# Kernel tuning notes

Measured on AMD Instinct MI355X. Metric: run time of the kernel, lower is better.

Reference implementation:

```python
import jax, jax.numpy as jnp
import numpy as np

B, T, J = 8, 1024, 25
D_MODEL, D_STATE, D_CONV, EXPAND = 256, 16, 4, 2
D_INNER = EXPAND * D_MODEL            # 512
DT_RANK = (D_MODEL + 15) // 16        # 16
N_CLASSES = 60


def layernorm(x, g, b, eps=1e-5):
    mu = x.mean(-1, keepdims=True)
    var = ((x - mu) ** 2).mean(-1, keepdims=True)
    return (x - mu) * jax.lax.rsqrt(var + eps) * g + b


def selective_scan(u, delta, A, Bm, Cm, D):
    # u, delta: [b,l,d]; A: [d,n]; Bm, Cm: [b,l,n]; D: [d]
    dA = jnp.exp(delta[..., None] * A)                              # [b,l,d,n]
    dBu = delta[..., None] * Bm[:, :, None, :] * u[..., None]        # [b,l,d,n]

    def step(h, inp):
        dA_t, dBu_t, C_t = inp
        h = dA_t * h + dBu_t                                         # [b,d,n]
        y = jnp.einsum('bdn,bn->bd', h, C_t)
        return h, y

    h0 = jnp.zeros((u.shape[0], u.shape[2], A.shape[1]), u.dtype)
    _, ys = jax.lax.scan(step, h0, (jnp.moveaxis(dA, 1, 0),
                                    jnp.moveaxis(dBu, 1, 0),
                                    jnp.moveaxis(Cm, 1, 0)))
    return jnp.moveaxis(ys, 0, 1) + u * D                            # [b,l,d]


def setup_inputs() -> dict:
    key = jax.random.key(0)
    ks = jax.random.split(key, 12)
    rn = lambda k, s, sc=0.02: jax.random.normal(k, s, jnp.float32) * sc
    A_log = jnp.log(jnp.tile(jnp.arange(1, D_STATE + 1, dtype=jnp.float32), (D_INNER, 1)))
    return {
        'x': jax.random.normal(ks[0], (B, T, J, 3), jnp.float32),
        'embed_w': rn(ks[1], (D_MODEL, J * 9)), 'embed_b': jnp.zeros((D_MODEL,), jnp.float32),
        'pre_g': jnp.ones((D_MODEL,), jnp.float32), 'pre_b': jnp.zeros((D_MODEL,), jnp.float32),
        'in_proj_w': rn(ks[2], (2 * D_INNER, D_MODEL)),
        'conv_w': rn(ks[3], (D_INNER, 1, D_CONV)), 'conv_b': jnp.zeros((D_INNER,), jnp.float32),
        'x_proj_w': rn(ks[4], (DT_RANK + 2 * D_STATE, D_INNER)),
        'dt_proj_w': rn(ks[5], (D_INNER, DT_RANK)), 'dt_proj_b': rn(ks[6], (D_INNER,), 0.1),
        'A_log': A_log, 'D': jnp.ones((D_INNER,), jnp.float32),
        'out_proj_w': rn(ks[7], (D_MODEL, D_INNER)),
        'post_g': jnp.ones((D_MODEL,), jnp.float32), 'post_b': jnp.zeros((D_MODEL,), jnp.float32),
        'fine_w': rn(ks[8], (N_CLASSES, D_MODEL)), 'fine_b': jnp.zeros((N_CLASSES,), jnp.float32),
    }


def reference(x, embed_w, embed_b, pre_g, pre_b, in_proj_w, conv_w, conv_b,
              x_proj_w, dt_proj_w, dt_proj_b, A_log, D, out_proj_w,
              post_g, post_b, fine_w, fine_b):
    b, t = x.shape[0], x.shape[1]
    # --- SkeletonNormalizer: root-center (scale_joints=None) ---
    pos = x[..., :3] - x[:, :, 0:1, :3]                              # [B,T,J,3]
    # --- MotionFeatureBuilder: pos / vel / acc ---
    vel = jnp.concatenate([jnp.zeros_like(pos[:, :1]), pos[:, 1:] - pos[:, :-1]], axis=1)
    acc = jnp.concatenate([jnp.zeros_like(vel[:, :1]), vel[:, 1:] - vel[:, :-1]], axis=1)
    feat = jnp.concatenate([pos, vel, acc], axis=-1).reshape(b, t, -1)  # [B,T,J*9]
    # --- embed ---
    feat = feat @ embed_w.T + embed_b                                # [B,T,D_MODEL]
    # --- Mamba block on pre-norm, residual add ---
    hn = layernorm(feat, pre_g, pre_b)
    xz = hn @ in_proj_w.T                                            # [B,T,2*D_INNER]
    xm, res = jnp.split(xz, 2, axis=-1)
    # depthwise causal conv1d over time
    xm = jax.lax.conv_general_dilated(
        jnp.swapaxes(xm, 1, 2), conv_w, (1,), [(D_CONV - 1, 0)],
        dimension_numbers=('NCH', 'OIH', 'NCH'), feature_group_count=D_INNER)
    xm = jnp.swapaxes(xm + conv_b[None, :, None], 1, 2)              # [B,T,D_INNER]
    xm = jax.nn.silu(xm)
    dbl = xm @ x_proj_w.T                                            # [B,T,DT_RANK+2*D_STATE]
    dt = dbl[..., :DT_RANK]
    Bm = dbl[..., DT_RANK:DT_RANK + D_STATE]
    Cm = dbl[..., DT_RANK + D_STATE:]
    delta = jax.nn.softplus(dt @ dt_proj_w.T + dt_proj_b)            # [B,T,D_INNER]
    A = -jnp.exp(A_log)                                              # [D_INNER,D_STATE]
    y = selective_scan(xm, delta, A, Bm, Cm, D)
    y = y * jax.nn.silu(res)
    y = y @ out_proj_w.T                                             # [B,T,D_MODEL]
    feat = feat + y
    # --- post norm, mean pool, classify ---
    feat = layernorm(feat, post_g, post_b)
    pooled = feat.mean(axis=1)                                       # [B,D_MODEL]
    return pooled @ fine_w.T + fine_b                                # [B,N_CLASSES]
```

## Files before the change

### kernel.cpp

```cpp
#include <hip/hip_runtime.h>
#include <hip/hip_bf16.h>
#include <math.h>

#define Bb 8
#define Tt 1024
#define Jj 25
#define D_MODEL 256
#define D_STATE 16
#define D_CONV 4
#define D_INNER 512
#define DT_RANK 16
#define N_CLASSES 60
#define Mrows (Bb*Tt)
#define NC 64
#define CL 16

typedef unsigned short u16;
using bf16x8 = __attribute__((ext_vector_type(8))) __bf16;
using f32x4  = __attribute__((ext_vector_type(4))) float;

__device__ inline u16 f2bf(float x) {
    unsigned u = __float_as_uint(x);
    unsigned r = (u + 0x7fffu + ((u >> 16) & 1u)) >> 16;
    return (u16)r;
}
__device__ inline float bf2f(u16 h) { return __uint_as_float((unsigned)h << 16); }
__device__ inline void split2(float x, u16& h, u16& l) {
    h = f2bf(x);
    l = f2bf(x - bf2f(h));
}
__device__ inline float softplus_fast(float s) {
    return fmaxf(s, 0.f) + __logf(1.f + __expf(-fabsf(s)));
}
__device__ inline f32x4 mfma3(bf16x8 ah, bf16x8 al, bf16x8 bh, bf16x8 bl, f32x4 c) {
    c = __builtin_amdgcn_mfma_f32_16x16x32_bf16(al, bh, c, 0, 0, 0);
    c = __builtin_amdgcn_mfma_f32_16x16x32_bf16(ah, bl, c, 0, 0, 0);
    c = __builtin_amdgcn_mfma_f32_16x16x32_bf16(ah, bh, c, 0, 0, 0);
    return c;
}

__global__ __launch_bounds__(256) void prep_kernel(
    const float* __restrict__ ew, const float* __restrict__ iw,
    const float* __restrict__ xw, const float* __restrict__ ow,
    u16* __restrict__ ebh, u16* __restrict__ ebl,
    u16* __restrict__ iph, u16* __restrict__ ipl,
    u16* __restrict__ xph, u16* __restrict__ xpl,
    u16* __restrict__ oph, u16* __restrict__ opl,
    float* __restrict__ blockpart) {
    int blk = blockIdx.x;
    if (blk < 1888) {
        int i = blk * 256 + threadIdx.x;
        const float* src; u16 *dh, *dl; int K, kshift, idx;
        if (i < 65536)       { src = ew; dh = ebh; dl = ebl; K = 225; kshift = 8; idx = i; }
        else if (i < 327680) { src = iw; dh = iph; dl = ipl; K = 256; kshift = 8; idx = i - 65536; }
        else if (i < 352256) { src = xw; dh = xph; dl = xpl; K = 512; kshift = 9; idx = i - 327680; }
        else                 { src = ow; dh = oph; dl = opl; K = 512; kshift = 9; idx = i - 352256; }
        int n = idx >> kshift;
        int k = idx & ((1 << kshift) - 1);
        float v = (k < K) ? src[(long)n * K + k] : 0.f;
        u16 h, l;
        split2(v, h, l);
        dh[idx] = h;
        dl[idx] = l;
    } else {
        int i = (blk - 1888) * 256 + threadIdx.x;
        blockpart[i] = 0.f;
    }
}

__global__ __launch_bounds__(512) void embed_ln_kernel(
    const float* __restrict__ x,
    const u16* __restrict__ Whi, const u16* __restrict__ Wlo,
    const float* __restrict__ bias,
    const float* __restrict__ g, const float* __restrict__ b,
    float* __restrict__ feat, u16* __restrict__ hnh, u16* __restrict__ hnl)
{
    constexpr int BM = 32, SW = 264;
    __shared__ u16 AsH[BM * SW], AsL[BM * SW];
    __shared__ float red[BM * 8];
    __shared__ float mu_s[BM], rs_s[BM];
    int tid = threadIdx.x;
    int m0 = blockIdx.x * BM;
    int lane = tid & 63, wave = tid >> 6;
    int fr = lane & 15, quad = lane >> 4;

    for (int s = tid; s < BM * 256; s += 512) {
        int row = s >> 8;
        int c = s & 255;
        float v = 0.f;
        if (c < 225) {
            long r = m0 + row;
            int t = (int)(r & (Tt - 1));
            int j = c / 9;
            int cc = c - j * 9;
            int comp = cc % 3;
            int kind = cc / 3;
            const float* pr = x + r * (Jj * 3);
            auto POS = [&](int dt) -> float {
                const float* p = pr - dt * (Jj * 3);
                return p[j * 3 + comp] - p[comp];
            };
            if (kind == 0) v = POS(0);
            else if (kind == 1) v = (t >= 1) ? (POS(0) - POS(1)) : 0.f;
            else {
                if (t >= 2)      v = POS(0) - 2.f * POS(1) + POS(2);
                else if (t == 1) v = POS(0) - POS(1);
                else             v = 0.f;
            }
        }
        u16 h, l;
        split2(v, h, l);
        AsH[row * SW + c] = h;
        AsL[row * SW + c] = l;
    }
    __syncthreads();

    f32x4 acc[2][2] = {};
    int nb = wave * 32;
#pragma unroll
    for (int k0 = 0; k0 < 256; k0 += 32) {
        bf16x8 aH[2], aL[2], bH[2], bL[2];
#pragma unroll
        for (int im = 0; im < 2; im++) {
            int r = im * 16 + fr;
            aH[im] = *(const bf16x8*)&AsH[r * SW + k0 + quad * 8];
            aL[im] = *(const bf16x8*)&AsL[r * SW + k0 + quad * 8];
        }
#pragma unroll
        for (int in = 0; in < 2; in++) {
            long off = (long)(nb + in * 16 + fr) * 256 + k0 + quad * 8;
            bH[in] = *(const bf16x8*)(Whi + off);
            bL[in] = *(const bf16x8*)(Wlo + off);
        }
#pragma unroll
        for (int im = 0; im < 2; im++)
#pragma unroll
            for (int in = 0; in < 2; in++)
                acc[im][in] = mfma3(aH[im], aL[im], bH[in], bL[in], acc[im][in]);
    }

    float bias_c[2], g_c[2], b_c[2];
#pragma unroll
    for (int in = 0; in < 2; in++) {
        int gn = nb + in * 16 + fr;
        bias_c[in] = bias[gn];
        g_c[in] = g[gn];
        b_c[in] = b[gn];
    }
#pragma unroll
    for (int im = 0; im < 2; im++)
#pragma unroll
        for (int in = 0; in < 2; in++)
#pragma unroll
            for (int reg = 0; reg < 4; reg++) {
                float v = acc[im][in][reg] + bias_c[in];
                acc[im][in][reg] = v;
                int gm = m0 + im * 16 + quad * 4 + reg;
                int gn = nb + in * 16 + fr;
                feat[(long)gm * 256 + gn] = v;
            }
#pragma unroll
    for (int im = 0; im < 2; im++)
#pragma unroll
        for (int reg = 0; reg < 4; reg++) {
            float p = acc[im][0][reg] + acc[im][1][reg];
            p += __shfl_xor(p, 1);
            p += __shfl_xor(p, 2);
            p += __shfl_xor(p, 4);
            p += __shfl_xor(p, 8);
            if (fr == 0) red[(im * 16 + quad * 4 + reg) * 8 + wave] = p;
        }
    __syncthreads();
    if (tid < BM) {
        float s = 0.f;
#pragma unroll
        for (int i = 0; i < 8; i++) s += red[tid * 8 + i];
        mu_s[tid] = s * (1.f / 256.f);
    }
    __syncthreads();
#pragma unroll
    for (int im = 0; im < 2; im++)
#pragma unroll
        for (int reg = 0; reg < 4; reg++) {
            int rl = im * 16 + quad * 4 + reg;
            float m = mu_s[rl];
            float d0 = acc[im][0][reg] - m, d1 = acc[im][1][reg] - m;
            float p = d0 * d0 + d1 * d1;
            p += __shfl_xor(p, 1);
            p += __shfl_xor(p, 2);
            p += __shfl_xor(p, 4);
            p += __shfl_xor(p, 8);
            if (fr == 0) red[rl * 8 + wave] = p;
        }
    __syncthreads();
    if (tid < BM) {
        float s = 0.f;
#pragma unroll
        for (int i = 0; i < 8; i++) s += red[tid * 8 + i];
        rs_s[tid] = rsqrtf(s * (1.f / 256.f) + 1e-5f);
    }
    __syncthreads();
#pragma unroll
    for (int im = 0; im < 2; im++)
#pragma unroll
        for (int in = 0; in < 2; in++)
#pragma unroll
            for (int reg = 0; reg < 4; reg++) {
                int rl = im * 16 + quad * 4 + reg;
                int gm = m0 + rl;
                int gn = nb + in * 16 + fr;
                float o = (acc[im][in][reg] - mu_s[rl]) * rs_s[rl] * g_c[in] + b_c[in];
                u16 hh, ll;
                split2(o, hh, ll);
                hnh[(long)gm * 256 + gn] = hh;
                hnl[(long)gm * 256 + gn] = ll;
            }
}

__global__ __launch_bounds__(512) void outproj_ln_pool_kernel(
    const u16* __restrict__ Ahi, const u16* __restrict__ Alo,
    const u16* __restrict__ Whi, const u16* __restrict__ Wlo,
    const float* __restrict__ resid,
    const float* __restrict__ g, const float* __restrict__ b,
    float* __restrict__ bp)
{
    constexpr int BM = 32, SW = 520;
    __shared__ u16 AsH[BM * SW], AsL[BM * SW];
    __shared__ float red[BM * 8];
    __shared__ float mu_s[BM], rs_s[BM];
    int tid = threadIdx.x;
    int m0 = blockIdx.x * BM;
    int lane = tid & 63, wave = tid >> 6;
    int fr = lane & 15, quad = lane >> 4;

    for (int s = tid; s < BM * 64; s += 512) {
        int row = s >> 6, seg = s & 63;
        long off = (long)(m0 + row) * 512 + seg * 8;
        *(uint4*)&AsH[row * SW + seg * 8] = *(const uint4*)(Ahi + off);
        *(uint4*)&AsL[row * SW + seg * 8] = *(const uint4*)(Alo + off);
    }
    __syncthreads();

    f32x4 acc[2][2] = {};
    int nb = wave * 32;
#pragma unroll 4
    for (int k0 = 0; k0 < 512; k0 += 32) {
        bf16x8 aH[2], aL[2], bH[2], bL[2];
#pragma unroll
        for (int im = 0; im < 2; im++) {
            int r = im * 16 + fr;
            aH[im] = *(const bf16x8*)&AsH[r * SW + k0 + quad * 8];
            aL[im] = *(const bf16x8*)&AsL[r * SW + k0 + quad * 8];
        }
#pragma unroll
        for (int in = 0; in < 2; in++) {
            long off = (long)(nb + in * 16 + fr) * 512 + k0 + quad * 8;
            bH[in] = *(const bf16x8*)(Whi + off);
            bL[in] = *(const bf16x8*)(Wlo + off);
        }
#pragma unroll
        for (int im = 0; im < 2; im++)
#pragma unroll
            for (int in = 0; in < 2; in++)
                acc[im][in] = mfma3(aH[im], aL[im], bH[in], bL[in], acc[im][in]);
    }

    float g_c[2], b_c[2];
#pragma unroll
    for (int in = 0; in < 2; in++) {
        int gn = nb + in * 16 + fr;
        g_c[in] = g[gn];
        b_c[in] = b[gn];
    }
#pragma unroll
    for (int im = 0; im < 2; im++)
#pragma unroll
        for (int in = 0; in < 2; in++)
#pragma unroll
            for (int reg = 0; reg < 4; reg++) {
                int gm = m0 + im * 16 + quad * 4 + reg;
                int gn = nb + in * 16 + fr;
                acc[im][in][reg] += resid[(long)gm * 256 + gn];
            }
#pragma unroll
    for (int im = 0; im < 2; im++)
#pragma unroll
        for (int reg = 0; reg < 4; reg++) {
            float p = acc[im][0][reg] + acc[im][1][reg];
            p += __shfl_xor(p, 1);
            p += __shfl_xor(p, 2);
            p += __shfl_xor(p, 4);
            p += __shfl_xor(p, 8);
            if (fr == 0) red[(im * 16 + quad * 4 + reg) * 8 + wave] = p;
        }
    __syncthreads();
    if (tid < BM) {
        float s = 0.f;
#pragma unroll
        for (int i = 0; i < 8; i++) s += red[tid * 8 + i];
        mu_s[tid] = s * (1.f / 256.f);
    }
    __syncthreads();
#pragma unroll
    for (int im = 0; im < 2; im++)
#pragma unroll
        for (int reg = 0; reg < 4; reg++) {
            int rl = im * 16 + quad * 4 + reg;
            float m = mu_s[rl];
            float d0 = acc[im][0][reg] - m, d1 = acc[im][1][reg] - m;
            float p = d0 * d0 + d1 * d1;
            p += __shfl_xor(p, 1);
            p += __shfl_xor(p, 2);
            p += __shfl_xor(p, 4);
            p += __shfl_xor(p, 8);
            if (fr == 0) red[rl * 8 + wave] = p;
        }
    __syncthreads();
    if (tid < BM) {
        float s = 0.f;
#pragma unroll
        for (int i = 0; i < 8; i++) s += red[tid * 8 + i];
        rs_s[tid] = rsqrtf(s * (1.f / 256.f) + 1e-5f);
    }
    __syncthreads();
#pragma unroll
    for (int in = 0; in < 2; in++) {
        float cs = 0.f;
#pragma unroll
        for (int im = 0; im < 2; im++)
#pragma unroll
            for (int reg = 0; reg < 4; reg++) {
                int rl = im * 16 + quad * 4 + reg;
                cs += (acc[im][in][reg] - mu_s[rl]) * rs_s[rl] * g_c[in] + b_c[in];
            }
        cs += __shfl_xor(cs, 16);
        cs += __shfl_xor(cs, 32);
        if (quad == 0) {
            int gn = nb + in * 16 + fr;
            atomicAdd(&bp[(long)(m0 >> 6) * 256 + gn], cs);
        }
    }
}

template<int BM, int BN, int EPI>
__global__ __launch_bounds__(256) void gemm_mfma(
    const u16* __restrict__ Ahi, const u16* __restrict__ Alo, int lda,
    const u16* __restrict__ Whi, const u16* __restrict__ Wlo, int ldw,
    const float* __restrict__ bias, const float* __restrict__ resid, int ldr,
    float* __restrict__ C, int ldc, int M, int N, int K)
{
    constexpr int TM = BM / 32;
    constexpr int TN = BN / 32;
    constexpr int SA = 40;
    __shared__ u16 AsH[BM * SA], AsL[BM * SA];
    __shared__ u16 WsH[BN * SA], WsL[BN * SA];
    int tid = threadIdx.x;
    int m0 = blockIdx.y * BM;
    int n0 = blockIdx.x * BN;
    int lane = tid & 63;
    int wave = tid >> 6;
    int wm = wave >> 1, wn = wave & 1;
    int fr = lane & 15, quad = lane >> 4;
    f32x4 acc[TM][TN] = {};

    for (int k0 = 0; k0 < K; k0 += 32) {
        for (int s = tid; s < BM * 4; s += 256) {
            int row = s >> 2, seg = s & 3;
            long off = (long)(m0 + row) * lda + k0 + seg * 8;
            *(uint4*)&AsH[row * SA + seg * 8] = *(const uint4*)(Ahi + off);
            *(uint4*)&AsL[row * SA + seg * 8] = *(const uint4*)(Alo + off);
        }
        for (int s = tid; s < BN * 4; s += 256) {
            int row = s >> 2, seg = s & 3;
            long off = (long)(n0 + row) * ldw + k0 + seg * 8;
            *(uint4*)&WsH[row * SA + seg * 8] = *(const uint4*)(Whi + off);
            *(uint4*)&WsL[row * SA + seg * 8] = *(const uint4*)(Wlo + off);
        }
        __syncthreads();
        bf16x8 aH[TM], aL[TM], bH[TN], bL[TN];
#pragma unroll
        for (int im = 0; im < TM; im++) {
            int r = wm * (BM / 2) + im * 16 + fr;
            aH[im] = *(const bf16x8*)&AsH[r * SA + quad * 8];
            aL[im] = *(const bf16x8*)&AsL[r * SA + quad * 8];
        }
#pragma unroll
        for (int in = 0; in < TN; in++) {
            int r = wn * (BN / 2) + in * 16 + fr;
            bH[in] = *(const bf16x8*)&WsH[r * SA + quad * 8];
            bL[in] = *(const bf16x8*)&WsL[r * SA + quad * 8];
        }
#pragma unroll
        for (int im = 0; im < TM; im++)
#pragma unroll
            for (int in = 0; in < TN; in++)
                acc[im][in] = mfma3(aH[im], aL[im], bH[in], bL[in], acc[im][in]);
        __syncthreads();
    }
#pragma unroll
    for (int im = 0; im < TM; im++) {
#pragma unroll
        for (int in = 0; in < TN; in++) {
#pragma unroll
            for (int reg = 0; reg < 4; reg++) {
                int gm = m0 + wm * (BM / 2) + im * 16 + quad * 4 + reg;
                int gn = n0 + wn * (BN / 2) + in * 16 + fr;
                float v = acc[im][in][reg];
                if (EPI == 1) v += bias[gn];
                if (EPI == 3) v += resid[(long)gm * ldr + gn];
                C[(long)gm * ldc + gn] = v;
            }
        }
    }
}

__global__ __launch_bounds__(256) void conv_xproj_kernel(
    const float* __restrict__ xz,
    const float* __restrict__ cw, const float* __restrict__ cb,
    const u16* __restrict__ Whi, const u16* __restrict__ Wlo,
    u16* __restrict__ xmh, u16* __restrict__ xml,
    float* __restrict__ dbl)
{
    constexpr int SA = 40;
    __shared__ u16 AsH[16 * SA], AsL[16 * SA];
    __shared__ u16 WsH[64 * SA], WsL[64 * SA];
    int tid = threadIdx.x;
    int m0 = blockIdx.x * 16;
    int lane = tid & 63, wave = tid >> 6;
    int fr = lane & 15, quad = lane >> 4;
    f32x4 acc = {};

    if (tid < 64) {
        int wr = 48 + (tid >> 2), seg = tid & 3;
        *(uint4*)&WsH[wr * SA + seg * 8] = make_uint4(0, 0, 0, 0);
        *(uint4*)&WsL[wr * SA + seg * 8] = make_uint4(0, 0, 0, 0);
    }

    int row = tid >> 4;
    int cg  = tid & 15;
    long gr = m0 + row;
    int t = gr & (Tt - 1);
    const float* xzr = xz + gr * 1024;

    for (int k0 = 0; k0 < 512; k0 += 32) {
        int c0 = k0 + cg * 2;
        float2 x0 = *(const float2*)(xzr + c0);
        float2 x1 = (t >= 1) ? *(const float2*)(xzr - 1024 + c0) : make_float2(0, 0);
        float2 x2 = (t >= 2) ? *(const float2*)(xzr - 2048 + c0) : make_float2(0, 0);
        float2 x3 = (t >= 3) ? *(const float2*)(xzr - 3072 + c0) : make_float2(0, 0);
        u16 hh0, ll0, hh1, ll1;
        {
            float4 w = *(const float4*)(cw + (c0 + 0) * 4);
            float a = cb[c0 + 0] + w.w * x0.x + w.z * x1.x + w.y * x2.x + w.x * x3.x;
            float s = a / (1.f + __expf(-a));
            split2(s, hh0, ll0);
            w = *(const float4*)(cw + (c0 + 1) * 4);
            a = cb[c0 + 1] + w.w * x0.y + w.z * x1.y + w.y * x2.y + w.x * x3.y;
            s = a / (1.f + __expf(-a));
            split2(s, hh1, ll1);
        }
        unsigned ph = hh0 | ((unsigned)hh1 << 16);
        unsigned pl = ll0 | ((unsigned)ll1 << 16);
        *(unsigned*)(xmh + gr * 512 + c0) = ph;
        *(unsigned*)(xml + gr * 512 + c0) = pl;
        *(unsigned*)&AsH[row * SA + cg * 2] = ph;
        *(unsigned*)&AsL[row * SA + cg * 2] = pl;
        if (tid < 192) {
            int wr = tid >> 2, seg = tid & 3;
            long off = (long)wr * 512 + k0 + seg * 8;
            *(uint4*)&WsH[wr * SA + seg * 8] = *(const uint4*)(Whi + off);
            *(uint4*)&WsL[wr * SA + seg * 8] = *(const uint4*)(Wlo + off);
        }
        __syncthreads();
        bf16x8 aH = *(const bf16x8*)&AsH[fr * SA + quad * 8];
        bf16x8 aL = *(const bf16x8*)&AsL[fr * SA + quad * 8];
        int wrow = wave * 16 + fr;
        bf16x8 bH = *(const bf16x8*)&WsH[wrow * SA + quad * 8];
        bf16x8 bL = *(const bf16x8*)&WsL[wrow * SA + quad * 8];
        acc = mfma3(aH, aL, bH, bL, acc);
        __syncthreads();
    }
    int gn = wave * 16 + fr;
    if (gn < 48) {
#pragma unroll
        for (int reg = 0; reg < 4; reg++) {
            int gm = m0 + quad * 4 + reg;
            dbl[(long)gm * 48 + gn] = acc[reg];
        }
    }
}

__global__ __launch_bounds__(512) void scan_p1(const float* __restrict__ dbl,
                                               const float* __restrict__ dtw,
                                               const float* __restrict__ dtb,
                                               const u16* __restrict__ xmh,
                                               const u16* __restrict__ xml,
                                               const float* __restrict__ A_log,
                                               float* __restrict__ chunkS,
                                               float* __restrict__ sumdelta) {
    __shared__ float ds[CL * 48];
    int b = blockIdx.x, c = blockIdx.y, d = threadIdx.x;
    long r0 = (long)b * Tt + (long)c * CL;
    for (int i = d; i < CL * 48; i += 512) ds[i] = dbl[r0 * 48 + i];

    float Arow[16];
#pragma unroll
    for (int n = 0; n < 16; n++) Arow[n] = -expf(A_log[d * 16 + n]);
    float4 wd[4];
#pragma unroll
    for (int q = 0; q < 4; q++) wd[q] = *(const float4*)(dtw + d * 16 + q * 4);
    float bdt = dtb[d];
    float S[16];
#pragma unroll
    for (int n = 0; n < 16; n++) S[n] = 0.f;
    float sd = 0.f;
    __syncthreads();

    for (int t = 0; t < CL; t++) {
        const float* row = ds + t * 48;
        float4 t0 = *(const float4*)(row + 0);
        float4 t1 = *(const float4*)(row + 4);
        float4 t2 = *(const float4*)(row + 8);
        float4 t3 = *(const float4*)(row + 12);
        float s = bdt;
        s += t0.x * wd[0].x + t0.y * wd[0].y + t0.z * wd[0].z + t0.w * wd[0].w;
        s += t1.x * wd[1].x + t1.y * wd[1].y + t1.z * wd[1].z + t1.w * wd[1].w;
        s += t2.x * wd[2].x + t2.y * wd[2].y + t2.z * wd[2].z + t2.w * wd[2].w;
        s += t3.x * wd[3].x + t3.y * wd[3].y + t3.z * wd[3].z + t3.w * wd[3].w;
        float dl = softplus_fast(s);
        long r = r0 + t;
        float u = bf2f(xmh[r * 512 + d]) + bf2f(xml[r * 512 + d]);
        float du = dl * u;
        sd += dl;
        float Bn[16];
#pragma unroll
        for (int q = 0; q < 4; q++) {
            float4 bv = *(const float4*)(row + 16 + q * 4);
            Bn[q*4+0] = bv.x; Bn[q*4+1] = bv.y; Bn[q*4+2] = bv.z; Bn[q*4+3] = bv.w;
        }
#pragma unroll
        for (int n = 0; n < 16; n++) {
            float a = __expf(dl * Arow[n]);
            S[n] = a * S[n] + du * Bn[n];
        }
    }
    long base = ((long)(b * NC + c) * 16) * 512 + d;
#pragma unroll
    for (int n = 0; n < 16; n++) chunkS[base + (long)n * 512] = S[n];
    sumdelta[(long)(b * NC + c) * 512 + d] = sd;
}

__global__ __launch_bounds__(256) void scan_combine(float* chunkS,
                                                    const float* __restrict__ sumdelta,
                                                    const float* __restrict__ A_log) {
    int idx = blockIdx.x * 256 + threadIdx.x;
    int d = idx & 511;
    int n = (idx >> 9) & 15;
    int b = idx >> 13;
    float Aval = -expf(A_log[d * 16 + n]);
    float h = 0.f;
    for (int c = 0; c < NC; c++) {
        long si = ((long)(b * NC + c) * 16 + n) * 512 + d;
        float s = chunkS[si];
        float a = __expf(Aval * sumdelta[(long)(b * NC + c) * 512 + d]);
        chunkS[si] = h;
        h = a * h + s;
    }
}

__global__ __launch_bounds__(512) void scan_p2(const float* __restrict__ dbl,
                                               const float* __restrict__ dtw,
                                               const float* __restrict__ dtb,
                                               const u16* xmh, const u16* xml,
                                               const float* __restrict__ xz,
                                               const float* __restrict__ A_log,
                                               const float* __restrict__ Dv,
                                               const float* __restrict__ chunkH,
                                               u16* yh, u16* yl) {
    __shared__ float ds[CL * 48];
    int b = blockIdx.x, c = blockIdx.y, d = threadIdx.x;
    long r0 = (long)b * Tt + (long)c * CL;
    for (int i = d; i < CL * 48; i += 512) ds[i] = dbl[r0 * 48 + i];

    float Arow[16];
#pragma unroll
    for (int n = 0; n < 16; n++) Arow[n] = -expf(A_log[d * 16 + n]);
    float4 wd[4];
#pragma unroll
    for (int q = 0; q < 4; q++) wd[q] = *(const float4*)(dtw + d * 16 + q * 4);
    float bdt = dtb[d];
    float Dd = Dv[d];
    float h[16];
    long base = ((long)(b * NC + c) * 16) * 512 + d;
#pragma unroll
    for (int n = 0; n < 16; n++) h[n] = chunkH[base + (long)n * 512];
    __syncthreads();

    for (int t = 0; t < CL; t++) {
        const float* row = ds + t * 48;
        float4 t0 = *(const float4*)(row + 0);
        float4 t1 = *(const float4*)(row + 4);
        float4 t2 = *(const float4*)(row + 8);
        float4 t3 = *(const float4*)(row + 12);
        float s = bdt;
        s += t0.x * wd[0].x + t0.y * wd[0].y + t0.z * wd[0].z + t0.w * wd[0].w;
        s += t1.x * wd[1].x + t1.y * wd[1].y + t1.z * wd[1].z + t1.w * wd[1].w;
        s += t2.x * wd[2].x + t2.y * wd[2].y + t2.z * wd[2].z + t2.w * wd[2].w;
        s += t3.x * wd[3].x + t3.y * wd[3].y + t3.z * wd[3].z + t3.w * wd[3].w;
        float dl = softplus_fast(s);
        long r = r0 + t;
        float u = bf2f(xmh[r * 512 + d]) + bf2f(xml[r * 512 + d]);
        float res = xz[r * 1024 + 512 + d];
        float du = dl * u;
        float Bn[16], Cn[16];
#pragma unroll
        for (int q = 0; q < 4; q++) {
            float4 bv = *(const float4*)(row + 16 + q * 4);
            float4 cv = *(const float4*)(row + 32 + q * 4);
            Bn[q*4+0] = bv.x; Bn[q*4+1] = bv.y; Bn[q*4+2] = bv.z; Bn[q*4+3] = bv.w;
            Cn[q*4+0] = cv.x; Cn[q*4+1] = cv.y; Cn[q*4+2] = cv.z; Cn[q*4+3] = cv.w;
        }
        float ysum = 0.f;
#pragma unroll
        for (int n = 0; n < 16; n++) {
            float a = __expf(dl * Arow[n]);
            h[n] = a * h[n] + du * Bn[n];
            ysum += h[n] * Cn[n];
        }
        float yy = ysum + u * Dd;
        float sres = res / (1.f + __expf(-res));
        float outv = yy * sres;
        u16 hh, ll;
        split2(outv, hh, ll);
        yh[r * 512 + d] = hh;
        yl[r * 512 + d] = ll;
    }
}

__global__ __launch_bounds__(256) void head_kernel(const float* __restrict__ bp,
                                                   const float* __restrict__ fw,
                                                   const float* __restrict__ fb,
                                                   float* __restrict__ out) {
    __shared__ float pld[256];
    int b = blockIdx.x;
    int d = threadIdx.x;
    float s = 0.f;
#pragma unroll
    for (int i = 0; i < 16; i++)
        s += bp[(long)(b * 16 + i) * 256 + d];
    pld[d] = s;
    __syncthreads();
    if (d < N_CLASSES) {
        float acc = 0.f;
        for (int k = 0; k < 256; k++) acc += pld[k] * fw[d * 256 + k];
        out[b * N_CLASSES + d] = acc * (1.f / (float)Tt) + fb[d];
    }
}

extern "C" void kernel_launch(void* const* d_in, const int* in_sizes, int n_in,
                              void* d_out, int out_size, void* d_ws, size_t ws_size,
                              hipStream_t stream) {
    const float* x         = (const float*)d_in[0];
    const float* embed_w   = (const float*)d_in[1];
    const float* embed_b   = (const float*)d_in[2];
    const float* pre_g     = (const float*)d_in[3];
    const float* pre_b     = (const float*)d_in[4];
    const float* in_proj_w = (const float*)d_in[5];
    const float* conv_w    = (const float*)d_in[6];
    const float* conv_b    = (const float*)d_in[7];
    const float* x_proj_w  = (const float*)d_in[8];
    const float* dt_proj_w = (const float*)d_in[9];
    const float* dt_proj_b = (const float*)d_in[10];
    const float* A_log     = (const float*)d_in[11];
    const float* Dv        = (const float*)d_in[12];
    const float* out_proj_w= (const float*)d_in[13];
    const float* post_g    = (const float*)d_in[14];
    const float* post_b    = (const float*)d_in[15];
    const float* fine_w    = (const float*)d_in[16];
    const float* fine_b    = (const float*)d_in[17];
    float* out = (float*)d_out;
    char* base = (char*)d_ws;

    float* feat     = (float*)(base + 0);
    float* xz       = (float*)(base + 8388608);
    float* chunkS   = (float*)(base + 41943040);
    u16*   xmh      = (u16*)  (base + 58720256);
    u16*   xml      = (u16*)  (base + 67108864);
    u16*   fbh      = (u16*)  (base + 75497472);
    u16*   fbl      = (u16*)  (base + 79691776);
    float* dbl      = (float*)(base + 83886080);
    float* sumdelta = (float*)(base + 85458944);
    float* blockpart= (float*)(base + 86507520);
    u16*   ebh      = (u16*)  (base + 86638592);
    u16*   ebl      = ebh + 65536;
    u16*   iph      = ebl + 65536;
    u16*   ipl      = iph + 262144;
    u16*   xph      = ipl + 262144;
    u16*   xpl      = xph + 24576;
    u16*   oph      = xpl + 24576;
    u16*   opl      = oph + 131072;

    prep_kernel<<<dim3(1888 + 128), dim3(256), 0, stream>>>(
        embed_w, in_proj_w, x_proj_w, out_proj_w,
        ebh, ebl, iph, ipl, xph, xpl, oph, opl, blockpart);

    embed_ln_kernel<<<dim3(Mrows / 32), dim3(512), 0, stream>>>(
        x, ebh, ebl, embed_b, pre_g, pre_b, feat, fbh, fbl);

    gemm_mfma<128,64,0><<<dim3(16, 64), dim3(256), 0, stream>>>(
        fbh, fbl, 256, iph, ipl, 256, nullptr, nullptr, 0, xz, 1024, Mrows, 1024, 256);

    conv_xproj_kernel<<<dim3(Mrows / 16), dim3(256), 0, stream>>>(
        xz, conv_w, conv_b, xph, xpl, xmh, xml, dbl);

    scan_p1<<<dim3(Bb, NC), dim3(512), 0, stream>>>(
        dbl, dt_proj_w, dt_proj_b, xmh, xml, A_log, chunkS, sumdelta);
    scan_combine<<<dim3(256), dim3(256), 0, stream>>>(chunkS, sumdelta, A_log);
    scan_p2<<<dim3(Bb, NC), dim3(512), 0, stream>>>(
        dbl, dt_proj_w, dt_proj_b, xmh, xml, xz, A_log, Dv, chunkS, xmh, xml);

    outproj_ln_pool_kernel<<<dim3(Mrows / 32), dim3(512), 0, stream>>>(
        xmh, xml, oph, opl, feat, post_g, post_b, blockpart);

    head_kernel<<<dim3(Bb), dim3(256), 0, stream>>>(blockpart, fine_w, fine_b, out);
}
```

Before: 247.6 us.

## Fuse embedding+LayerNorm with in_proj GEMM into a single kernel

The embed+pre-LN kernel now writes its normalized bf16 hi/lo tile into shared memory and immediately runs the in_proj GEMM (256→1024) on it. Each wave computes 128 output columns, reading the weights directly from global memory, and writes xz. This removes the separate gemm_mfma launch and the global round trip of the normalized activations. In exchange, each block rereads the full in_proj weights with no LDS staging, and the larger accumulator array raises register pressure under launch_bounds(512,2).

```diff
diff --git a/kernel.cpp b/kernel.cpp
--- a/kernel.cpp
+++ b/kernel.cpp
@@ -68,12 +68,13 @@
     }
 }
 
-__global__ __launch_bounds__(512) void embed_ln_kernel(
+__global__ __launch_bounds__(512, 2) void embed_inproj_kernel(
     const float* __restrict__ x,
-    const u16* __restrict__ Whi, const u16* __restrict__ Wlo,
+    const u16* __restrict__ Ehi, const u16* __restrict__ Elo,
     const float* __restrict__ bias,
     const float* __restrict__ g, const float* __restrict__ b,
-    float* __restrict__ feat, u16* __restrict__ hnh, u16* __restrict__ hnl)
+    const u16* __restrict__ Phi, const u16* __restrict__ Plo,
+    float* __restrict__ feat, float* __restrict__ xz)
 {
     constexpr int BM = 32, SW = 264;
     __shared__ u16 AsH[BM * SW], AsL[BM * SW];
@@ -115,8 +116,8 @@
     }
     __syncthreads();
 
-    f32x4 acc[2][2] = {};
-    int nb = wave * 32;
+    f32x4 acc1[2][2] = {};
+    int nb1 = wave * 32;
 #pragma unroll
     for (int k0 = 0; k0 < 256; k0 += 32) {
         bf16x8 aH[2], aL[2], bH[2], bL[2];
@@ -128,21 +129,21 @@
         }
 #pragma unroll
         for (int in = 0; in < 2; in++) {
-            long off = (long)(nb + in * 16 + fr) * 256 + k0 + quad * 8;
-            bH[in] = *(const bf16x8*)(Whi + off);
-            bL[in] = *(const bf16x8*)(Wlo + off);
+            long off = (long)(nb1 + in * 16 + fr) * 256 + k0 + quad * 8;
+            bH[in] = *(const bf16x8*)(Ehi + off);
+            bL[in] = *(const bf16x8*)(Elo + off);
         }
 #pragma unroll
         for (int im = 0; im < 2; im++)
 #pragma unroll
             for (int in = 0; in < 2; in++)
-                acc[im][in] = mfma3(aH[im], aL[im], bH[in], bL[in], acc[im][in]);
+                acc1[im][in] = mfma3(aH[im], aL[im], bH[in], bL[in], acc1[im][in]);
     }
 
     float bias_c[2], g_c[2], b_c[2];
 #pragma unroll
     for (int in = 0; in < 2; in++) {
-        int gn = nb + in * 16 + fr;
+        int gn = nb1 + in * 16 + fr;
         bias_c[in] = bias[gn];
         g_c[in] = g[gn];
         b_c[in] = b[gn];
@@ -153,17 +154,17 @@
         for (int in = 0; in < 2; in++)
 #pragma unroll
             for (int reg = 0; reg < 4; reg++) {
-                float v = acc[im][in][reg] + bias_c[in];
-                acc[im][in][reg] = v;
+                float v = acc1[im][in][reg] + bias_c[in];
+                acc1[im][in][reg] = v;
                 int gm = m0 + im * 16 + quad * 4 + reg;
-                int gn = nb + in * 16 + fr;
+                int gn = nb1 + in * 16 + fr;
                 feat[(long)gm * 256 + gn] = v;
             }
 #pragma unroll
     for (int im = 0; im < 2; im++)
 #pragma unroll
         for (int reg = 0; reg < 4; reg++) {
-            float p = acc[im][0][reg] + acc[im][1][reg];
+            float p = acc1[im][0][reg] + acc1[im][1][reg];
             p += __shfl_xor(p, 1);
             p += __shfl_xor(p, 2);
             p += __shfl_xor(p, 4);
@@ -184,7 +185,7 @@
         for (int reg = 0; reg < 4; reg++) {
             int rl = im * 16 + quad * 4 + reg;
             float m = mu_s[rl];
-            float d0 = acc[im][0][reg] - m, d1 = acc[im][1][reg] - m;
+            float d0 = acc1[im][0][reg] - m, d1 = acc1[im][1][reg] - m;
             float p = d0 * d0 + d1 * d1;
             p += __shfl_xor(p, 1);
             p += __shfl_xor(p, 2);
@@ -200,6 +201,7 @@
         rs_s[tid] = rsqrtf(s * (1.f / 256.f) + 1e-5f);
     }
     __syncthreads();
+
 #pragma unroll
     for (int im = 0; im < 2; im++)
 #pragma unroll
@@ -207,13 +209,45 @@
 #pragma unroll
             for (int reg = 0; reg < 4; reg++) {
                 int rl = im * 16 + quad * 4 + reg;
-                int gm = m0 + rl;
-                int gn = nb + in * 16 + fr;
-                float o = (acc[im][in][reg] - mu_s[rl]) * rs_s[rl] * g_c[in] + b_c[in];
+                int gn = nb1 + in * 16 + fr;
+                float o = (acc1[im][in][reg] - mu_s[rl]) * rs_s[rl] * g_c[in] + b_c[in];
                 u16 hh, ll;
                 split2(o, hh, ll);
-                hnh[(long)gm * 256 + gn] = hh;
-                hnl[(long)gm * 256 + gn] = ll;
+                AsH[rl * SW + gn] = hh;
+                AsL[rl * SW + gn] = ll;
+            }
+    __syncthreads();
+
+    f32x4 acc2[2][8] = {};
+    int nb2 = wave * 128;
+#pragma unroll 2
+    for (int k0 = 0; k0 < 256; k0 += 32) {
+        bf16x8 aH[2], aL[2];
+#pragma unroll
+        for (int im = 0; im < 2; im++) {
+            int r = im * 16 + fr;
+            aH[im] = *(const bf16x8*)&AsH[r * SW + k0 + quad * 8];
+            aL[im] = *(const bf16x8*)&AsL[r * SW + k0 + quad * 8];
+        }
+#pragma unroll
+        for (int in = 0; in < 8; in++) {
+            long off = (long)(nb2 + in * 16 + fr) * 256 + k0 + quad * 8;
+            bf16x8 bH = *(const bf16x8*)(Phi + off);
+            bf16x8 bL = *(const bf16x8*)(Plo + off);
+#pragma unroll
+            for (int im = 0; im < 2; im++)
+                acc2[im][in] = mfma3(aH[im], aL[im], bH, bL, acc2[im][in]);
+        }
+    }
+#pragma unroll
+    for (int im = 0; im < 2; im++)
+#pragma unroll
+        for (int in = 0; in < 8; in++)
+#pragma unroll
+            for (int reg = 0; reg < 4; reg++) {
+                int gm = m0 + im * 16 + quad * 4 + reg;
+                int gn = nb2 + in * 16 + fr;
+                xz[(long)gm * 1024 + gn] = acc2[im][in][reg];
             }
 }
 
@@ -338,78 +372,6 @@
         if (quad == 0) {
             int gn = nb + in * 16 + fr;
             atomicAdd(&bp[(long)(m0 >> 6) * 256 + gn], cs);
-        }
-    }
-}
-
-template<int BM, int BN, int EPI>
-__global__ __launch_bounds__(256) void gemm_mfma(
-    const u16* __restrict__ Ahi, const u16* __restrict__ Alo, int lda,
-    const u16* __restrict__ Whi, const u16* __restrict__ Wlo, int ldw,
-    const float* __restrict__ bias, const float* __restrict__ resid, int ldr,
-    float* __restrict__ C, int ldc, int M, int N, int K)
-{
-    constexpr int TM = BM / 32;
-    constexpr int TN = BN / 32;
-    constexpr int SA = 40;
-    __shared__ u16 AsH[BM * SA], AsL[BM * SA];
-    __shared__ u16 WsH[BN * SA], WsL[BN * SA];
-    int tid = threadIdx.x;
-    int m0 = blockIdx.y * BM;
-    int n0 = blockIdx.x * BN;
-    int lane = tid & 63;
-    int wave = tid >> 6;
-    int wm = wave >> 1, wn = wave & 1;
-    int fr = lane & 15, quad = lane >> 4;
-    f32x4 acc[TM][TN] = {};
-
-    for (int k0 = 0; k0 < K; k0 += 32) {
-        for (int s = tid; s < BM * 4; s += 256) {
-            int row = s >> 2, seg = s & 3;
-            long off = (long)(m0 + row) * lda + k0 + seg * 8;
-            *(uint4*)&AsH[row * SA + seg * 8] = *(const uint4*)(Ahi + off);
-            *(uint4*)&AsL[row * SA + seg * 8] = *(const uint4*)(Alo + off);
-        }
-        for (int s = tid; s < BN * 4; s += 256) {
-            int row = s >> 2, seg = s & 3;
-            long off = (long)(n0 + row) * ldw + k0 + seg * 8;
-            *(uint4*)&WsH[row * SA + seg * 8] = *(const uint4*)(Whi + off);
-            *(uint4*)&WsL[row * SA + seg * 8] = *(const uint4*)(Wlo + off);
-        }
-        __syncthreads();
-        bf16x8 aH[TM], aL[TM], bH[TN], bL[TN];
-#pragma unroll
-        for (int im = 0; im < TM; im++) {
-            int r = wm * (BM / 2) + im * 16 + fr;
-            aH[im] = *(const bf16x8*)&AsH[r * SA + quad * 8];
-            aL[im] = *(const bf16x8*)&AsL[r * SA + quad * 8];
-        }
-#pragma unroll
-        for (int in = 0; in < TN; in++) {
-            int r = wn * (BN / 2) + in * 16 + fr;
-            bH[in] = *(const bf16x8*)&WsH[r * SA + quad * 8];
-            bL[in] = *(const bf16x8*)&WsL[r * SA + quad * 8];
-        }
-#pragma unroll
-        for (int im = 0; im < TM; im++)
-#pragma unroll
-            for (int in = 0; in < TN; in++)
-                acc[im][in] = mfma3(aH[im], aL[im], bH[in], bL[in], acc[im][in]);
-        __syncthreads();
-    }
-#pragma unroll
-    for (int im = 0; im < TM; im++) {
-#pragma unroll
-        for (int in = 0; in < TN; in++) {
-#pragma unroll
-            for (int reg = 0; reg < 4; reg++) {
-                int gm = m0 + wm * (BM / 2) + im * 16 + quad * 4 + reg;
-                int gn = n0 + wn * (BN / 2) + in * 16 + fr;
-                float v = acc[im][in][reg];
-                if (EPI == 1) v += bias[gn];
-                if (EPI == 3) v += resid[(long)gm * ldr + gn];
-                C[(long)gm * ldc + gn] = v;
-            }
         }
     }
 }
@@ -686,8 +648,6 @@
     float* chunkS   = (float*)(base + 41943040);
     u16*   xmh      = (u16*)  (base + 58720256);
     u16*   xml      = (u16*)  (base + 67108864);
-    u16*   fbh      = (u16*)  (base + 75497472);
-    u16*   fbl      = (u16*)  (base + 79691776);
     float* dbl      = (float*)(base + 83886080);
     float* sumdelta = (float*)(base + 85458944);
     float* blockpart= (float*)(base + 86507520);
@@ -704,11 +664,8 @@
         embed_w, in_proj_w, x_proj_w, out_proj_w,
         ebh, ebl, iph, ipl, xph, xpl, oph, opl, blockpart);
 
-    embed_ln_kernel<<<dim3(Mrows / 32), dim3(512), 0, stream>>>(
-        x, ebh, ebl, embed_b, pre_g, pre_b, feat, fbh, fbl);
-
-    gemm_mfma<128,64,0><<<dim3(16, 64), dim3(256), 0, stream>>>(
-        fbh, fbl, 256, iph, ipl, 256, nullptr, nullptr, 0, xz, 1024, Mrows, 1024, 256);
+    embed_inproj_kernel<<<dim3(Mrows / 32), dim3(512), 0, stream>>>(
+        x, ebh, ebl, embed_b, pre_g, pre_b, iph, ipl, feat, xz);
 
     conv_xproj_kernel<<<dim3(Mrows / 16), dim3(256), 0, stream>>>(
         xz, conv_w, conv_b, xph, xpl, xmh, xml, dbl);
```

Result: slower. 257.7 us (+4.1%).

## Fuse causal conv, SiLU and x_proj GEMM into both chunked scan passes

Applied to the files above, without the earlier changes.

Removes the separate conv_xproj kernel. Each scan pass now recomputes the depthwise causal conv and SiLU for its 16-timestep chunk into shared memory, then runs the x_proj MFMA on three waves to build the dt/B/C rows locally. This drops the global round trips for xm (hi/lo bf16) and dbl, plus one launch. In exchange the conv and x_proj work is done twice (once per pass), shared memory per block grows, and only 3 of 8 waves do the GEMM while the rest wait at a barrier.

```diff
diff --git a/kernel.cpp b/kernel.cpp
--- a/kernel.cpp
+++ b/kernel.cpp
@@ -414,95 +414,40 @@
     }
 }
 
-__global__ __launch_bounds__(256) void conv_xproj_kernel(
+__global__ __launch_bounds__(512) void scan_p1f(
     const float* __restrict__ xz,
     const float* __restrict__ cw, const float* __restrict__ cb,
     const u16* __restrict__ Whi, const u16* __restrict__ Wlo,
-    u16* __restrict__ xmh, u16* __restrict__ xml,
-    float* __restrict__ dbl)
+    const float* __restrict__ dtw, const float* __restrict__ dtb,
+    const float* __restrict__ A_log,
+    float* __restrict__ chunkS, float* __restrict__ sumdelta)
 {
-    constexpr int SA = 40;
-    __shared__ u16 AsH[16 * SA], AsL[16 * SA];
-    __shared__ u16 WsH[64 * SA], WsL[64 * SA];
-    int tid = threadIdx.x;
-    int m0 = blockIdx.x * 16;
-    int lane = tid & 63, wave = tid >> 6;
-    int fr = lane & 15, quad = lane >> 4;
-    f32x4 acc = {};
-
-    if (tid < 64) {
-        int wr = 48 + (tid >> 2), seg = tid & 3;
-        *(uint4*)&WsH[wr * SA + seg * 8] = make_uint4(0, 0, 0, 0);
-        *(uint4*)&WsL[wr * SA + seg * 8] = make_uint4(0, 0, 0, 0);
-    }
-
-    int row = tid >> 4;
-    int cg  = tid & 15;
-    long gr = m0 + row;
-    int t = gr & (Tt - 1);
-    const float* xzr = xz + gr * 1024;
-
-    for (int k0 = 0; k0 < 512; k0 += 32) {
-        int c0 = k0 + cg * 2;
-        float2 x0 = *(const float2*)(xzr + c0);
-        float2 x1 = (t >= 1) ? *(const float2*)(xzr - 1024 + c0) : make_float2(0, 0);
-        float2 x2 = (t >= 2) ? *(const float2*)(xzr - 2048 + c0) : make_float2(0, 0);
-        float2 x3 = (t >= 3) ? *(const float2*)(xzr - 3072 + c0) : make_float2(0, 0);
-        u16 hh0, ll0, hh1, ll1;
-        {
-            float4 w = *(const float4*)(cw + (c0 + 0) * 4);
-            float a = cb[c0 + 0] + w.w * x0.x + w.z * x1.x + w.y * x2.x + w.x * x3.x;
-            float s = a / (1.f + __expf(-a));
-            split2(s, hh0, ll0);
-            w = *(const float4*)(cw + (c0 + 1) * 4);
-            a = cb[c0 + 1] + w.w * x0.y + w.z * x1.y + w.y * x2.y + w.x * x3.y;
-            s = a / (1.f + __expf(-a));
-            split2(s, hh1, ll1);
-        }
-        unsigned ph = hh0 | ((unsigned)hh1 << 16);
-        unsigned pl = ll0 | ((unsigned)ll1 << 16);
-        *(unsigned*)(xmh + gr * 512 + c0) = ph;
-        *(unsigned*)(xml + gr * 512 + c0) = pl;
-        *(unsigned*)&AsH[row * SA + cg * 2] = ph;
-        *(unsigned*)&AsL[row * SA + cg * 2] = pl;
-        if (tid < 192) {
-            int wr = tid >> 2, seg = tid & 3;
-            long off = (long)wr * 512 + k0 + seg * 8;
-            *(uint4*)&WsH[wr * SA + seg * 8] = *(const uint4*)(Whi + off);
-            *(uint4*)&WsL[wr * SA + seg * 8] = *(const uint4*)(Wlo + off);
-        }
-        __syncthreads();
-        bf16x8 aH = *(const bf16x8*)&AsH[fr * SA + quad * 8];
-        bf16x8 aL = *(const bf16x8*)&AsL[fr * SA + quad * 8];
-        int wrow = wave * 16 + fr;
-        bf16x8 bH = *(const bf16x8*)&WsH[wrow * SA + quad * 8];
-        bf16x8 bL = *(const bf16x8*)&WsL[wrow * SA + quad * 8];
-        acc = mfma3(aH, aL, bH, bL, acc);
-        __syncthreads();
-    }
-    int gn = wave * 16 + fr;
-    if (gn < 48) {
-#pragma unroll
-        for (int reg = 0; reg < 4; reg++) {
-            int gm = m0 + quad * 4 + reg;
-            dbl[(long)gm * 48 + gn] = acc[reg];
-        }
-    }
-}
-
-__global__ __launch_bounds__(512) void scan_p1(const float* __restrict__ dbl,
-                                               const float* __restrict__ dtw,
-                                               const float* __restrict__ dtb,
-                                               const u16* __restrict__ xmh,
-                                               const u16* __restrict__ xml,
-                                               const float* __restrict__ A_log,
-                                               float* __restrict__ chunkS,
-                                               float* __restrict__ sumdelta) {
+    constexpr int SW = 520;
+    __shared__ u16 AsH[CL * SW], AsL[CL * SW];
     __shared__ float ds[CL * 48];
     int b = blockIdx.x, c = blockIdx.y, d = threadIdx.x;
+    int lane = d & 63, wave = d >> 6;
+    int fr = lane & 15, quad = lane >> 4;
     long r0 = (long)b * Tt + (long)c * CL;
-    for (int i = d; i < CL * 48; i += 512) ds[i] = dbl[r0 * 48 + i];
-
+    int t0 = c * CL;
+
+    float4 w4 = *(const float4*)(cw + d * 4);
+    float cbd = cb[d];
+    const float* xc = xz + r0 * 1024 + d;
+    float h1 = (t0 >= 1) ? xc[-1024] : 0.f;
+    float h2 = (t0 >= 2) ? xc[-2048] : 0.f;
+    float h3 = (t0 >= 3) ? xc[-3072] : 0.f;
+#pragma unroll
+    for (int t = 0; t < CL; t++) {
+        float cur = xc[t * 1024];
+        float a = cbd + w4.w * cur + w4.z * h1 + w4.y * h2 + w4.x * h3;
+        float s = a / (1.f + __expf(-a));
+        u16 hh, ll;
+        split2(s, hh, ll);
+        AsH[t * SW + d] = hh;
+        AsL[t * SW + d] = ll;
+        h3 = h2; h2 = h1; h1 = cur;
+    }
     float Arow[16];
 #pragma unroll
     for (int n = 0; n < 16; n++) Arow[n] = -expf(A_log[d * 16 + n]);
@@ -510,26 +455,42 @@
 #pragma unroll
     for (int q = 0; q < 4; q++) wd[q] = *(const float4*)(dtw + d * 16 + q * 4);
     float bdt = dtb[d];
+    __syncthreads();
+
+    if (wave < 3) {
+        f32x4 acc = {};
+#pragma unroll
+        for (int k0 = 0; k0 < 512; k0 += 32) {
+            bf16x8 aH = *(const bf16x8*)&AsH[fr * SW + k0 + quad * 8];
+            bf16x8 aL = *(const bf16x8*)&AsL[fr * SW + k0 + quad * 8];
+            long off = (long)(wave * 16 + fr) * 512 + k0 + quad * 8;
+            bf16x8 bH = *(const bf16x8*)(Whi + off);
+            bf16x8 bL = *(const bf16x8*)(Wlo + off);
+            acc = mfma3(aH, aL, bH, bL, acc);
+        }
+#pragma unroll
+        for (int reg = 0; reg < 4; reg++)
+            ds[(quad * 4 + reg) * 48 + wave * 16 + fr] = acc[reg];
+    }
+    __syncthreads();
+
     float S[16];
 #pragma unroll
     for (int n = 0; n < 16; n++) S[n] = 0.f;
     float sd = 0.f;
-    __syncthreads();
-
     for (int t = 0; t < CL; t++) {
         const float* row = ds + t * 48;
-        float4 t0 = *(const float4*)(row + 0);
-        float4 t1 = *(const float4*)(row + 4);
-        float4 t2 = *(const float4*)(row + 8);
-        float4 t3 = *(const float4*)(row + 12);
+        float4 t1 = *(const float4*)(row + 0);
+        float4 t2 = *(const float4*)(row + 4);
+        float4 t3 = *(const float4*)(row + 8);
+        float4 t4 = *(const float4*)(row + 12);
         float s = bdt;
-        s += t0.x * wd[0].x + t0.y * wd[0].y + t0.z * wd[0].z + t0.w * wd[0].w;
-        s += t1.x * wd[1].x + t1.y * wd[1].y + t1.z * wd[1].z + t1.w * wd[1].w;
-        s += t2.x * wd[2].x + t2.y * wd[2].y + t2.z * wd[2].z + t2.w * wd[2].w;
-        s += t3.x * wd[3].x + t3.y * wd[3].y + t3.z * wd[3].z + t3.w * wd[3].w;
+        s += t1.x * wd[0].x + t1.y * wd[0].y + t1.z * wd[0].z + t1.w * wd[0].w;
+        s += t2.x * wd[1].x + t2.y * wd[1].y + t2.z * wd[1].z + t2.w * wd[1].w;
+        s += t3.x * wd[2].x + t3.y * wd[2].y + t3.z * wd[2].z + t3.w * wd[2].w;
+        s += t4.x * wd[3].x + t4.y * wd[3].y + t4.z * wd[3].z + t4.w * wd[3].w;
         float dl = softplus_fast(s);
-        long r = r0 + t;
-        float u = bf2f(xmh[r * 512 + d]) + bf2f(xml[r * 512 + d]);
+        float u = bf2f(AsH[t * SW + d]) + bf2f(AsL[t * SW + d]);
         float du = dl * u;
         sd += dl;
         float Bn[16];
@@ -568,20 +529,41 @@
     }
 }
 
-__global__ __launch_bounds__(512) void scan_p2(const float* __restrict__ dbl,
-                                               const float* __restrict__ dtw,
-                                               const float* __restrict__ dtb,
-                                               const u16* xmh, const u16* xml,
-                                               const float* __restrict__ xz,
-                                               const float* __restrict__ A_log,
-                                               const float* __restrict__ Dv,
-                                               const float* __restrict__ chunkH,
-                                               u16* yh, u16* yl) {
+__global__ __launch_bounds__(512) void scan_p2f(
+    const float* __restrict__ xz,
+    const float* __restrict__ cw, const float* __restrict__ cb,
+    const u16* __restrict__ Whi, const u16* __restrict__ Wlo,
+    const float* __restrict__ dtw, const float* __restrict__ dtb,
+    const float* __restrict__ A_log, const float* __restrict__ Dv,
+    const float* __restrict__ chunkH,
+    u16* __restrict__ yh, u16* __restrict__ yl)
+{
+    constexpr int SW = 520;
+    __shared__ u16 AsH[CL * SW], AsL[CL * SW];
     __shared__ float ds[CL * 48];
     int b = blockIdx.x, c = blockIdx.y, d = threadIdx.x;
+    int lane = d & 63, wave = d >> 6;
+    int fr = lane & 15, quad = lane >> 4;
     long r0 = (long)b * Tt + (long)c * CL;
-    for (int i = d; i < CL * 48; i += 512) ds[i] = dbl[r0 * 48 + i];
-
+    int t0 = c * CL;
+
+    float4 w4 = *(const float4*)(cw + d * 4);
+    float cbd = cb[d];
+    const float* xc = xz + r0 * 1024 + d;
+    float h1 = (t0 >= 1) ? xc[-1024] : 0.f;
+    float h2 = (t0 >= 2) ? xc[-2048] : 0.f;
+    float h3 = (t0 >= 3) ? xc[-3072] : 0.f;
+#pragma unroll
+    for (int t = 0; t < CL; t++) {
+        float cur = xc[t * 1024];
+        float a = cbd + w4.w * cur + w4.z * h1 + w4.y * h2 + w4.x * h3;
+        float s = a / (1.f + __expf(-a));
+        u16 hh, ll;
+        split2(s, hh, ll);
+        AsH[t * SW + d] = hh;
+        AsL[t * SW + d] = ll;
+        h3 = h2; h2 = h1; h1 = cur;
+    }
     float Arow[16];
 #pragma unroll
     for (int n = 0; n < 16; n++) Arow[n] = -expf(A_log[d * 16 + n]);
@@ -596,21 +578,38 @@
     for (int n = 0; n < 16; n++) h[n] = chunkH[base + (long)n * 512];
     __syncthreads();
 
+    if (wave < 3) {
+        f32x4 acc = {};
+#pragma unroll
+        for (int k0 = 0; k0 < 512; k0 += 32) {
+            bf16x8 aH = *(const bf16x8*)&AsH[fr * SW + k0 + quad * 8];
+            bf16x8 aL = *(const bf16x8*)&AsL[fr * SW + k0 + quad * 8];
+            long off = (long)(wave * 16 + fr) * 512 + k0 + quad * 8;
+            bf16x8 bH = *(const bf16x8*)(Whi + off);
+            bf16x8 bL = *(const bf16x8*)(Wlo + off);
+            acc = mfma3(aH, aL, bH, bL, acc);
+        }
+#pragma unroll
+        for (int reg = 0; reg < 4; reg++)
+            ds[(quad * 4 + reg) * 48 + wave * 16 + fr] = acc[reg];
+    }
+    __syncthreads();
+
+    const float* xres = xz + r0 * 1024 + 512 + d;
     for (int t = 0; t < CL; t++) {
         const float* row = ds + t * 48;
-        float4 t0 = *(const float4*)(row + 0);
-        float4 t1 = *(const float4*)(row + 4);
-        float4 t2 = *(const float4*)(row + 8);
-        float4 t3 = *(const float4*)(row + 12);
+        float4 t1 = *(const float4*)(row + 0);
+        float4 t2 = *(const float4*)(row + 4);
+        float4 t3 = *(const float4*)(row + 8);
+        float4 t4 = *(const float4*)(row + 12);
         float s = bdt;
-        s += t0.x * wd[0].x + t0.y * wd[0].y + t0.z * wd[0].z + t0.w * wd[0].w;
-        s += t1.x * wd[1].x + t1.y * wd[1].y + t1.z * wd[1].z + t1.w * wd[1].w;
-        s += t2.x * wd[2].x + t2.y * wd[2].y + t2.z * wd[2].z + t2.w * wd[2].w;
-        s += t3.x * wd[3].x + t3.y * wd[3].y + t3.z * wd[3].z + t3.w * wd[3].w;
+        s += t1.x * wd[0].x + t1.y * wd[0].y + t1.z * wd[0].z + t1.w * wd[0].w;
+        s += t2.x * wd[1].x + t2.y * wd[1].y + t2.z * wd[1].z + t2.w * wd[1].w;
+        s += t3.x * wd[2].x + t3.y * wd[2].y + t3.z * wd[2].z + t3.w * wd[2].w;
+        s += t4.x * wd[3].x + t4.y * wd[3].y + t4.z * wd[3].z + t4.w * wd[3].w;
         float dl = softplus_fast(s);
-        long r = r0 + t;
-        float u = bf2f(xmh[r * 512 + d]) + bf2f(xml[r * 512 + d]);
-        float res = xz[r * 1024 + 512 + d];
+        float u = bf2f(AsH[t * SW + d]) + bf2f(AsL[t * SW + d]);
+        float res = xres[t * 1024];
         float du = dl * u;
         float Bn[16], Cn[16];
 #pragma unroll
@@ -632,6 +631,7 @@
         float outv = yy * sres;
         u16 hh, ll;
         split2(outv, hh, ll);
+        long r = r0 + t;
         yh[r * 512 + d] = hh;
         yl[r * 512 + d] = ll;
     }
@@ -688,7 +688,6 @@
     u16*   xml      = (u16*)  (base + 67108864);
     u16*   fbh      = (u16*)  (base + 75497472);
     u16*   fbl      = (u16*)  (base + 79691776);
-    float* dbl      = (float*)(base + 83886080);
     float* sumdelta = (float*)(base + 85458944);
     float* blockpart= (float*)(base + 86507520);
     u16*   ebh      = (u16*)  (base + 86638592);
@@ -710,14 +709,13 @@
     gemm_mfma<128,64,0><<<dim3(16, 64), dim3(256), 0, stream>>>(
         fbh, fbl, 256, iph, ipl, 256, nullptr, nullptr, 0, xz, 1024, Mrows, 1024, 256);
 
-    conv_xproj_kernel<<<dim3(Mrows / 16), dim3(256), 0, stream>>>(
-        xz, conv_w, conv_b, xph, xpl, xmh, xml, dbl);
-
-    scan_p1<<<dim3(Bb, NC), dim3(512), 0, stream>>>(
-        dbl, dt_proj_w, dt_proj_b, xmh, xml, A_log, chunkS, sumdelta);
+    scan_p1f<<<dim3(Bb, NC), dim3(512), 0, stream>>>(
+        xz, conv_w, conv_b, xph, xpl, dt_proj_w, dt_proj_b, A_log,
+        chunkS, sumdelta);
     scan_combine<<<dim3(256), dim3(256), 0, stream>>>(chunkS, sumdelta, A_log);
-    scan_p2<<<dim3(Bb, NC), dim3(512), 0, stream>>>(
-        dbl, dt_proj_w, dt_proj_b, xmh, xml, xz, A_log, Dv, chunkS, xmh, xml);
+    scan_p2f<<<dim3(Bb, NC), dim3(512), 0, stream>>>(
+        xz, conv_w, conv_b, xph, xpl, dt_proj_w, dt_proj_b, A_log, Dv,
+        chunkS, xmh, xml);
 
     outproj_ln_pool_kernel<<<dim3(Mrows / 32), dim3(512), 0, stream>>>(
         xmh, xml, oph, opl, feat, post_g, post_b, blockpart);
```

Result: faster. 236.0 us (-4.7%).
